# Kernel optimization log

Measured on AMD Instinct MI355X. Metric: run time of the kernel, lower is better.

Reference implementation:

```python
import jax, jax.numpy as jnp
import numpy as np

B, N, QD = 2, 2048, 1024
HEADS, DIM_HEAD = 16, 64
INNER = HEADS * DIM_HEAD  # 1024
SCALE = DIM_HEAD ** -0.5


def setup_inputs() -> dict:
    key = jax.random.key(0)
    ks = jax.random.split(key, 8)
    x = jax.random.normal(ks[0], (B, N, QD), dtype=jnp.float32)
    bias = jax.random.normal(ks[1], (B, N, N), dtype=jnp.float32)
    mask = jax.random.randint(ks[2], (B, N), 0, 2) > 0
    # parameters (nn.Linear stores weight [out, in]; we keep [in, out] and matmul x @ W)
    Wq = jax.random.normal(ks[3], (QD, INNER), dtype=jnp.float32) * (QD ** -0.5)
    Wkv = jax.random.normal(ks[4], (QD, 2 * INNER), dtype=jnp.float32) * (QD ** -0.5)
    Wo = jax.random.normal(ks[5], (INNER, QD), dtype=jnp.float32) * (INNER ** -0.5)
    bo = jax.random.normal(ks[6], (QD,), dtype=jnp.float32) * 0.01
    return {"x": x, "bias": bias, "mask": mask, "Wq": Wq, "Wkv": Wkv, "Wo": Wo, "bo": bo}


def reference(x, bias, mask, Wq, Wkv, Wo, bo):
    b, n, _ = x.shape
    q = x @ Wq                      # [b, n, inner]
    kv = x @ Wkv                    # [b, n, 2*inner] (context defaults to x)
    k, v = jnp.split(kv, 2, axis=-1)
    # split heads: [b, h, n, d]
    split = lambda t: t.reshape(b, n, HEADS, DIM_HEAD).transpose(0, 2, 1, 3)
    q, k, v = split(q), split(k), split(v)
    sim = jnp.einsum('bhid,bhjd->bhij', q, k) * SCALE   # [b, h, n, n]
    sim = sim + bias[:, None, :, :]                      # additive bias broadcast over heads
    max_neg = -jnp.finfo(sim.dtype).max
    sim = jnp.where(mask[:, None, None, :], sim, max_neg)  # per-key mask
    attn = jax.nn.softmax(sim, axis=-1)
    out = jnp.einsum('bhij,bhjd->bhid', attn, v)         # [b, h, n, d]
    out = out.transpose(0, 2, 1, 3).reshape(b, n, INNER)  # merge heads
    return out @ Wo + bo
```

## Files before the change

### kernel.cpp

```cpp
#include <hip/hip_runtime.h>
#include <hip/hip_bf16.h>
#include <stdint.h>

#define B_     2
#define N_     2048
#define QD_    1024
#define H_     16
#define DH_    64
#define INNER_ 1024
#define SCALE_ 0.125f

typedef unsigned short u16;
typedef __attribute__((ext_vector_type(8))) short bf16x8;
typedef __attribute__((ext_vector_type(4))) float f32x4;
typedef __attribute__((ext_vector_type(4))) unsigned short u16x4;
typedef __attribute__((ext_vector_type(8))) unsigned short u16x8;

#define GLD16(gp, lp) __builtin_amdgcn_global_load_lds( \
    (const __attribute__((address_space(1))) unsigned int*)(gp), \
    (__attribute__((address_space(3))) unsigned int*)(lp), 16, 0, 0)

__device__ inline u16 f2bf(float f) {
    union { float f; uint32_t u; } c; c.f = f;
    uint32_t r = c.u + 0x7FFFu + ((c.u >> 16) & 1u);
    return (u16)(r >> 16);
}
__device__ inline float bf2f(u16 s) {
    union { uint32_t u; float f; } c; c.u = ((uint32_t)s) << 16;
    return c.f;
}
__device__ inline void split2(float v, u16 &h, u16 &l) {
    u16 hs = f2bf(v);
    h = hs;
    l = f2bf(v - bf2f(hs));
}
__device__ inline unsigned pk2(float a, float b) {
    float2 f; f.x = a; f.y = b;
    union { __hip_bfloat162 v; unsigned u; } c;
    c.v = __float22bfloat162_rn(f);
    return c.u;
}
__device__ inline float f4get(const float4& v, int r) {
    return r == 0 ? v.x : r == 1 ? v.y : r == 2 ? v.z : v.w;
}

__global__ __launch_bounds__(256) void prep_kernel(
    const float* __restrict__ x, u16* __restrict__ xh, u16* __restrict__ xl,
    const float* __restrict__ Wq, const float* __restrict__ Wkv, const float* __restrict__ Wo,
    u16* __restrict__ wTh, u16* __restrict__ wTl,
    u16* __restrict__ woTh, u16* __restrict__ woTl)
{
    __shared__ float t[32][33];
    const int blk = blockIdx.x, tid = threadIdx.x;
    if (blk < 4096) {
        int idx = blk * 256 + tid;
        float4 v = ((const float4*)x)[idx];
        u16x4 hv, lv; u16 h, l;
        split2(v.x, h, l); hv.x = h; lv.x = l;
        split2(v.y, h, l); hv.y = h; lv.y = l;
        split2(v.z, h, l); hv.z = h; lv.z = l;
        split2(v.w, h, l); hv.w = h; lv.w = l;
        ((u16x4*)xh)[idx] = hv;
        ((u16x4*)xl)[idx] = lv;
        return;
    }
    int local = blk - 4096;
    const float* src; u16 *dhi, *dlo; int C, bx, by;
    if (local < 1024)      { src = Wq;  dhi = wTh;                dlo = wTl;                C = 1024; by = local >> 5; bx = local & 31; }
    else if (local < 3072) { int l2 = local - 1024; src = Wkv; dhi = wTh + 1024 * 1024; dlo = wTl + 1024 * 1024; C = 2048; by = l2 >> 6; bx = l2 & 63; }
    else                   { int l2 = local - 3072; src = Wo;  dhi = woTh;               dlo = woTl;               C = 1024; by = l2 >> 5; bx = l2 & 31; }
    const int x0 = bx * 32, y0 = by * 32;
    const int tx = tid & 31, ty = tid >> 5;
    for (int yy = ty; yy < 32; yy += 8)
        t[yy][tx] = src[(size_t)(y0 + yy) * C + x0 + tx];
    __syncthreads();
    for (int i = ty; i < 32; i += 8) {
        float v = t[tx][i];
        u16 h, l; split2(v, h, l);
        size_t o = (size_t)(x0 + i) * 1024 + y0 + tx;
        dhi[o] = h; dlo[o] = l;
    }
}

__device__ inline void bias_read(int T, int bkoff, int bl16,
                                 const float* __restrict__ bias,
                                 const int* __restrict__ mask,
                                 float4 bR[4], int4& bM)
{
    int bb2 = T >> 10, rest = T & 1023;
    int k0b = (rest & 31) * 64, q0 = (rest >> 5) * 64;
    int kk = k0b + bkoff;
    bM = *(const int4*)&mask[bb2 * N_ + kk];
#pragma unroll
    for (int m = 0; m < 4; m++)
        bR[m] = *(const float4*)&bias[((size_t)bb2 * N_ + q0 + m * 16 + bl16) * N_ + kk];
}
__device__ inline void bias_store(int T, int bwvr, int blane, int bhf,
                                  const float4 bR[4], const int4& bM,
                                  u16* __restrict__ bsw)
{
    int bb2 = T >> 10, rest = T & 1023;
    int k0b = (rest & 31) * 64, q0 = (rest >> 5) * 64;
    int wv = ((k0b >> 5) & 3) + bwvr;
    const u16 NEG = f2bf(-1e30f);
    const int mok[4] = { bM.x, bM.y, bM.z, bM.w };
    u16x8 o0, o1;
#pragma unroll
    for (int i = 0; i < 8; i++) {
        int m = i >> 2, r = i & 3;
        o0[i] = mok[r] ? f2bf(f4get(bR[m], r)) : NEG;
    }
#pragma unroll
    for (int i = 0; i < 8; i++) {
        int m = 2 + (i >> 2), r = i & 3;
        o1[i] = mok[r] ? f2bf(f4get(bR[m], r)) : NEG;
    }
    size_t ob = ((((size_t)bb2 * 32 + (q0 >> 6)) * 16 + (k0b >> 7)) * 4 + wv) * 2048
                + (size_t)blane * 32 + bhf * 16;
    *(u16x8*)&bsw[ob]     = o0;
    *(u16x8*)&bsw[ob + 8] = o1;
}

__global__ __launch_bounds__(256) void bias_kernel(
    const float* __restrict__ bias, const int* __restrict__ mask,
    u16* __restrict__ bsw)
{
    const int bid = blockIdx.x, tid = threadIdx.x;
    const int bp = tid >> 1, bhf = tid & 1;
    const int blane = bp & 63, bquad = blane >> 4, bl16 = blane & 15;
    const int bwvr = bp >> 6;
    const int bkoff = bwvr * 32 + bquad * 8 + bhf * 4;
    float4 bR[4]; int4 bM;
    bias_read(bid, bkoff, bl16, bias, mask, bR, bM);
    bias_store(bid, bwvr, blane, bhf, bR, bM, bsw);
}

__global__ __launch_bounds__(256) void gemm_qkv(
    const u16* __restrict__ Ah, const u16* __restrict__ Al,
    const u16* __restrict__ Bh,
    u16* __restrict__ qh,
    u16* __restrict__ kb, u16* __restrict__ vT)
{
    __shared__ __align__(16) char smem[49152];
    const int tid = threadIdx.x;
    const int gid = blockIdx.x;

    const int wave = tid >> 6, lane = tid & 63;
    const int quad = lane >> 4, l16 = lane & 15;
    const int wm = wave >> 1, wn = wave & 1;
    const int bx = gid % 24, by = gid / 24;
    const int bm = by * 128, bn = bx * 128;
    const bool comp = (bx < 8);

    f32x4 acc[4][4];
#pragma unroll
    for (int i = 0; i < 4; i++)
#pragma unroll
        for (int j = 0; j < 4; j++) acc[i][j] = (f32x4){0.f, 0.f, 0.f, 0.f};

    const int row0 = tid >> 2, g4 = tid & 3;
    const int r1 = row0, r2 = row0 + 64;
    const int gc1 = (g4 ^ (r1 & 3)) * 8, gc2 = (g4 ^ (r2 & 3)) * 8;
    const size_t a1 = (size_t)(bm + r1) * 1024 + gc1, a2 = (size_t)(bm + r2) * 1024 + gc2;
    const size_t b1 = (size_t)(bn + r1) * 1024 + gc1, b2 = (size_t)(bn + r2) * 1024 + gc2;
    const int ldsw = wave * 1024;

    auto issue = [&](char* base, int kn) {
        GLD16(Ah + a1 + kn, base + ldsw);
        GLD16(Ah + a2 + kn, base + 4096 + ldsw);
        GLD16(Bh + b1 + kn, base + 16384 + ldsw);
        GLD16(Bh + b2 + kn, base + 20480 + ldsw);
        if (comp) {
            GLD16(Al + a1 + kn, base + 8192 + ldsw);
            GLD16(Al + a2 + kn, base + 12288 + ldsw);
        }
    };

    issue(smem, 0);
    int cur = 0;
    for (int k0 = 0; k0 < 1024; k0 += 32) {
        __syncthreads();
        char* cb_ = smem + cur * 24576;
        if (k0 + 32 < 1024) issue(smem + (cur ^ 1) * 24576, k0 + 32);
        const u16* cAh = (const u16*)cb_;
        const u16* cAl = (const u16*)(cb_ + 8192);
        const u16* cBh = (const u16*)(cb_ + 16384);
        bf16x8 fah[4], fal[4], fbh[4];
#pragma unroll
        for (int s = 0; s < 4; s++) {
            int ra = wm * 64 + s * 16 + l16;
            int rb = wn * 64 + s * 16 + l16;
            int ca = (quad ^ (ra & 3)) * 8;
            int cb = (quad ^ (rb & 3)) * 8;
            fah[s] = *(const bf16x8*)&cAh[ra * 32 + ca];
            fbh[s] = *(const bf16x8*)&cBh[rb * 32 + cb];
            if (comp) fal[s] = *(const bf16x8*)&cAl[ra * 32 + ca];
        }
#pragma unroll
        for (int sm = 0; sm < 4; sm++)
#pragma unroll
            for (int sn = 0; sn < 4; sn++) {
                acc[sm][sn] = __builtin_amdgcn_mfma_f32_16x16x32_bf16(fah[sm], fbh[sn], acc[sm][sn], 0, 0, 0);
                if (comp)
                    acc[sm][sn] = __builtin_amdgcn_mfma_f32_16x16x32_bf16(fal[sm], fbh[sn], acc[sm][sn], 0, 0, 0);
            }
        cur ^= 1;
    }
#pragma unroll
    for (int sm = 0; sm < 4; sm++) {
        int rowb = bm + wm * 64 + sm * 16 + quad * 4;
        int bb = rowb >> 11, i0 = rowb & 2047;
#pragma unroll
        for (int sn = 0; sn < 4; sn++) {
            int col = bn + wn * 64 + sn * 16 + l16;
            int region = col >> 10;
            int hh = (col >> 6) & 15;
            int d = col & 63;
            if (region == 0) {
#pragma unroll
                for (int r = 0; r < 4; r++) {
                    size_t o = (((size_t)(bb * H_ + hh)) * N_ + i0 + r) * DH_ + d;
                    qh[o] = f2bf(acc[sm][sn][r] * SCALE_);
                }
            } else if (region == 1) {
#pragma unroll
                for (int r = 0; r < 4; r++) {
                    size_t o = (((size_t)(bb * H_ + hh)) * N_ + i0 + r) * DH_ + d;
                    kb[o] = f2bf(acc[sm][sn][r]);
                }
            } else {
                u16x4 pv;
#pragma unroll
                for (int r = 0; r < 4; r++) pv[r] = f2bf(acc[sm][sn][r]);
                *(u16x4*)&vT[(((size_t)(bb * H_ + hh)) * DH_ + d) * N_ + i0] = pv;
            }
        }
    }
}

__global__ __launch_bounds__(256) void gemm_out(
    const u16* __restrict__ Ab,
    const u16* __restrict__ Bh,
    const float* __restrict__ bo, float* __restrict__ out)
{
    __shared__ __align__(16) char smem[24576];
    const int tid = threadIdx.x;
    const int wave = tid >> 6, lane = tid & 63;
    const int quad = lane >> 4, l16 = lane & 15;
    const int wm = wave >> 1, wn = wave & 1;
    const int bm = blockIdx.y * 128, bn = blockIdx.x * 64;

    f32x4 acc[4][2];
#pragma unroll
    for (int i = 0; i < 4; i++)
#pragma unroll
        for (int j = 0; j < 2; j++) acc[i][j] = (f32x4){0.f, 0.f, 0.f, 0.f};

    const int row0 = tid >> 2, g4 = tid & 3;
    const int r1 = row0, r2 = row0 + 64;
    const int gc1 = (g4 ^ (r1 & 3)) * 8, gc2 = (g4 ^ (r2 & 3)) * 8;
    const size_t a1 = (size_t)(bm + r1) * 1024 + gc1, a2 = (size_t)(bm + r2) * 1024 + gc2;
    const size_t bgo = (size_t)(bn + r1) * 1024 + gc1;
    const int ldsw = wave * 1024;

    auto issue = [&](char* base, int kn) {
        GLD16(Ab + a1 + kn, base + ldsw);
        GLD16(Ab + a2 + kn, base + 4096 + ldsw);
        GLD16(Bh + bgo + kn, base + 8192 + ldsw);
    };

    issue(smem, 0);
    int cur = 0;
    for (int k0 = 0; k0 < 1024; k0 += 32) {
        __syncthreads();
        char* cb_ = smem + cur * 12288;
        if (k0 + 32 < 1024) issue(smem + (cur ^ 1) * 12288, k0 + 32);
        const u16* cA  = (const u16*)cb_;
        const u16* cBh = (const u16*)(cb_ + 8192);
        bf16x8 fa[4], fbh[2];
#pragma unroll
        for (int s = 0; s < 4; s++) {
            int ra = wm * 64 + s * 16 + l16;
            int ca = (quad ^ (ra & 3)) * 8;
            fa[s] = *(const bf16x8*)&cA[ra * 32 + ca];
        }
#pragma unroll
        for (int s = 0; s < 2; s++) {
            int rb = wn * 32 + s * 16 + l16;
            int cb = (quad ^ (rb & 3)) * 8;
            fbh[s] = *(const bf16x8*)&cBh[rb * 32 + cb];
        }
#pragma unroll
        for (int sm = 0; sm < 4; sm++)
#pragma unroll
            for (int sn = 0; sn < 2; sn++)
                acc[sm][sn] = __builtin_amdgcn_mfma_f32_16x16x32_bf16(fa[sm], fbh[sn], acc[sm][sn], 0, 0, 0);
        cur ^= 1;
    }
#pragma unroll
    for (int sm = 0; sm < 4; sm++) {
        int rowb = bm + wm * 64 + sm * 16 + quad * 4;
#pragma unroll
        for (int sn = 0; sn < 2; sn++) {
            int col = bn + wn * 32 + sn * 16 + l16;
            float bv = bo[col];
#pragma unroll
            for (int r = 0; r < 4; r++)
                out[(size_t)(rowb + r) * 1024 + col] = acc[sm][sn][r] + bv;
        }
    }
}

#define LDK 72
#define LDV 128

__global__ __launch_bounds__(256, 2) void attn_kernel(
    const u16* __restrict__ qh,
    const u16* __restrict__ kb, const u16* __restrict__ vT,
    const u16* __restrict__ bsw, u16* __restrict__ ob)
{
    __shared__ __align__(16) char smem[35328];
    u16* sK  = (u16*)smem;
    u16* sVt = (u16*)(smem + 18432);
    float* rO = (float*)smem;
    float* rL = (float*)(smem + 34816);

    const int bh = blockIdx.y, b = bh >> 4, h = bh & 15;
    const int qt = blockIdx.x, qbase = qt * 64;
    const int tid = threadIdx.x, wave = tid >> 6, lane = tid & 63;
    const int quad = lane >> 4, l16 = lane & 15;

    bf16x8 aq[4][2];
#pragma unroll
    for (int m = 0; m < 4; m++) {
        size_t qo = ((size_t)bh * N_ + qbase + m * 16 + l16) * DH_ + quad * 8;
        aq[m][0] = *(const bf16x8*)&qh[qo];
        aq[m][1] = *(const bf16x8*)&qh[qo + 32];
    }
    f32x4 Oacc[4][4], lacc[4];
#pragma unroll
    for (int m = 0; m < 4; m++) {
        lacc[m] = (f32x4){0.f, 0.f, 0.f, 0.f};
#pragma unroll
        for (int nd = 0; nd < 4; nd++) Oacc[m][nd] = (f32x4){0.f, 0.f, 0.f, 0.f};
    }
    bf16x8 ones;
#pragma unroll
    for (int i = 0; i < 8; i++) ones[i] = (short)0x3F80;

    const int rK = tid >> 3, cK = (tid & 7) * 8;
    const int sigK = ((rK & 4) << 2) + ((rK >> 3) << 2) + (rK & 3);
    const int rV = tid >> 4;
    const int vg = tid & 15;
    const int cV = vg * 8;
    const int vsw = (vg ^ (rV & 7)) * 8;
    const int vrg = ((wave * 4 + quad) ^ (l16 & 7)) * 8;
    const size_t kgbase = (size_t)bh * N_ * DH_;
    const size_t vgbase = (size_t)bh * DH_ * N_;
    const size_t bswb = (size_t)(b * 32 + qt) * 131072 + (size_t)wave * 2048
                        + (size_t)lane * 32;

    bf16x8 pK[4], pV[4];
    u16x8 cB[4], nB[4];
#pragma unroll
    for (int it = 0; it < 4; it++) {
        pK[it] = *(const bf16x8*)&kb[kgbase + (size_t)(rK + it * 32) * DH_ + cK];
        pV[it] = *(const bf16x8*)&vT[vgbase + (size_t)(rV + it * 16) * N_ + cV];
    }
#pragma unroll
    for (int c = 0; c < 4; c++) cB[c] = *(const u16x8*)&bsw[bswb + c * 8];

    for (int jt = 0; jt < 16; jt++) {
#pragma unroll
        for (int it = 0; it < 4; it++) {
            *(bf16x8*)&sK[(it * 32 + sigK) * LDK + cK] = pK[it];
            *(bf16x8*)&sVt[(rV + it * 16) * LDV + vsw] = pV[it];
        }
        __syncthreads();
        {
            int jn = (jt + 1) & 15;
            int j0n = jn * 128;
#pragma unroll
            for (int it = 0; it < 4; it++) {
                pK[it] = *(const bf16x8*)&kb[kgbase + (size_t)(j0n + rK + it * 32) * DH_ + cK];
                pV[it] = *(const bf16x8*)&vT[vgbase + (size_t)(rV + it * 16) * N_ + j0n + cV];
            }
            size_t bb = bswb + (size_t)jn * 8192;
#pragma unroll
            for (int c = 0; c < 4; c++) nB[c] = *(const u16x8*)&bsw[bb + c * 8];
        }
        bf16x8 kf[2][2], vf[4];
#pragma unroll
        for (int n = 0; n < 2; n++)
#pragma unroll
            for (int s = 0; s < 2; s++)
                kf[n][s] = *(const bf16x8*)&sK[(wave * 32 + n * 16 + l16) * LDK + s * 32 + quad * 8];
#pragma unroll
        for (int nd = 0; nd < 4; nd++)
            vf[nd] = *(const bf16x8*)&sVt[(nd * 16 + l16) * LDV + vrg];

#pragma unroll
        for (int m = 0; m < 4; m++) {
            f32x4 S0 = (f32x4){0.f, 0.f, 0.f, 0.f};
            f32x4 S1 = (f32x4){0.f, 0.f, 0.f, 0.f};
#pragma unroll
            for (int s = 0; s < 2; s++) {
                S0 = __builtin_amdgcn_mfma_f32_16x16x32_bf16(kf[0][s], aq[m][s], S0, 0, 0, 0);
                S1 = __builtin_amdgcn_mfma_f32_16x16x32_bf16(kf[1][s], aq[m][s], S1, 0, 0, 0);
            }
            float p0[4], p1[4];
#pragma unroll
            for (int r = 0; r < 4; r++) {
                p0[r] = __expf(S0[r] + bf2f(cB[m >> 1][(m & 1) * 4 + r]));
                p1[r] = __expf(S1[r] + bf2f(cB[2 + (m >> 1)][(m & 1) * 4 + r]));
            }
            union { bf16x8 v; unsigned w[4]; } pa;
            pa.w[0] = pk2(p0[0], p0[1]);
            pa.w[1] = pk2(p0[2], p0[3]);
            pa.w[2] = pk2(p1[0], p1[1]);
            pa.w[3] = pk2(p1[2], p1[3]);
            lacc[m] = __builtin_amdgcn_mfma_f32_16x16x32_bf16(pa.v, ones, lacc[m], 0, 0, 0);
#pragma unroll
            for (int nd = 0; nd < 4; nd++)
                Oacc[m][nd] = __builtin_amdgcn_mfma_f32_16x16x32_bf16(pa.v, vf[nd], Oacc[m][nd], 0, 0, 0);
        }
#pragma unroll
        for (int c = 0; c < 4; c++) cB[c] = nB[c];
        __syncthreads();
    }

    if (wave >= 2) {
        int slot = wave - 2;
#pragma unroll
        for (int m = 0; m < 4; m++) {
#pragma unroll
            for (int nd = 0; nd < 4; nd++)
#pragma unroll
                for (int r = 0; r < 4; r++)
                    rO[(slot * 64 + m * 16 + quad * 4 + r) * 68 + nd * 16 + l16] = Oacc[m][nd][r];
            if (l16 == 0)
#pragma unroll
                for (int r = 0; r < 4; r++)
                    rL[slot * 64 + m * 16 + quad * 4 + r] = lacc[m][r];
        }
    }
    __syncthreads();
    if (wave < 2) {
        int slot = wave;
#pragma unroll
        for (int m = 0; m < 4; m++) {
#pragma unroll
            for (int nd = 0; nd < 4; nd++)
#pragma unroll
                for (int r = 0; r < 4; r++) {
                    int idx = (slot * 64 + m * 16 + quad * 4 + r) * 68 + nd * 16 + l16;
                    rO[idx] += Oacc[m][nd][r];
                }
            if (l16 == 0)
#pragma unroll
                for (int r = 0; r < 4; r++)
                    rL[slot * 64 + m * 16 + quad * 4 + r] += lacc[m][r];
        }
    }
    __syncthreads();
    {
        const int q = tid >> 2, dg = (tid & 3) * 16;
        float l = rL[q] + rL[64 + q];
        float inv = 1.f / l;
        f32x4 s[4];
#pragma unroll
        for (int i4 = 0; i4 < 4; i4++) {
            s[i4] = *(const f32x4*)&rO[(size_t)q * 68 + dg + i4 * 4];
            f32x4 v = *(const f32x4*)&rO[(size_t)(64 + q) * 68 + dg + i4 * 4];
            s[i4] += v;
        }
        size_t obase = ((size_t)b * N_ + qbase + q) * INNER_ + h * 64 + dg;
#pragma unroll
        for (int i4 = 0; i4 < 4; i4++) {
            u16x4 o4;
#pragma unroll
            for (int r = 0; r < 4; r++) o4[r] = f2bf(s[i4][r] * inv);
            *(u16x4*)&ob[obase + i4 * 4] = o4;
        }
    }
}

extern "C" void kernel_launch(void* const* d_in, const int* in_sizes, int n_in,
                              void* d_out, int out_size, void* d_ws, size_t ws_size,
                              hipStream_t stream)
{
    const float* x    = (const float*)d_in[0];
    const float* bias = (const float*)d_in[1];
    const int*   mask = (const int*)d_in[2];
    const float* Wq   = (const float*)d_in[3];
    const float* Wkv  = (const float*)d_in[4];
    const float* Wo   = (const float*)d_in[5];
    const float* bo   = (const float*)d_in[6];
    float* out = (float*)d_out;

    char* w = (char*)d_ws;
    const size_t MB = 1024 * 1024;
    u16* q_h   = (u16*)(w);
    u16* k_b   = (u16*)(w + 16 * MB);
    u16* v_T   = (u16*)(w + 24 * MB);
    u16* xs_h  = (u16*)(w + 32 * MB);
    u16* xs_l  = (u16*)(w + 40 * MB);
    u16* wT_h  = (u16*)(w + 48 * MB);
    u16* wT_l  = (u16*)(w + 54 * MB);
    u16* woT_h = (u16*)(w + 60 * MB);
    u16* woT_l = (u16*)(w + 62 * MB);
    u16* o_b   = (u16*)(w + 64 * MB);

    const size_t bsw_bytes = (size_t)2 * N_ * N_ * sizeof(u16);
    const bool concurrent = ws_size >= 72 * MB + bsw_bytes;

    u16* bsw = concurrent ? (u16*)(w + 72 * MB) : (u16*)(w + 32 * MB);

    prep_kernel<<<8192, 256, 0, stream>>>(x, xs_h, xs_l, Wq, Wkv, Wo, wT_h, wT_l, woT_h, woT_l);
    gemm_qkv<<<768, 256, 0, stream>>>(xs_h, xs_l, wT_h, q_h, k_b, v_T);
    bias_kernel<<<2048, 256, 0, stream>>>(bias, mask, bsw);
    attn_kernel<<<dim3(32, 32), 256, 0, stream>>>(q_h, k_b, v_T, bsw, o_b);
    gemm_out<<<dim3(16, 32), 256, 0, stream>>>(o_b, woT_h, bo, out);
}
```

Baseline: 269.5 us.

## Fuse bias prep into prep kernel and remap attention grid per XCD

When the workspace is large enough, the bias/mask conversion blocks are appended to the prep kernel, which removes one kernel launch and lets that work run alongside the input and weight splitting. The attention grid is flattened to 1D and remapped so each XCD handles four consecutive (batch, head) pairs, which should improve L2 reuse of K/V. The last iteration no longer prefetches a wrapped-around tile. In exchange the prep kernel gets longer, and the remapping assumes round-robin block dispatch across 8 XCDs.

Result: no change. 270.3 us (+0.3%).

```diff
diff --git a/kernel.cpp b/kernel.cpp
--- a/kernel.cpp
+++ b/kernel.cpp
@@ -44,14 +44,72 @@
     return r == 0 ? v.x : r == 1 ? v.y : r == 2 ? v.z : v.w;
 }
 
+__device__ inline void bias_read(int T, int bkoff, int bl16,
+                                 const float* __restrict__ bias,
+                                 const int* __restrict__ mask,
+                                 float4 bR[4], int4& bM)
+{
+    int bb2 = T >> 10, rest = T & 1023;
+    int k0b = (rest & 31) * 64, q0 = (rest >> 5) * 64;
+    int kk = k0b + bkoff;
+    bM = *(const int4*)&mask[bb2 * N_ + kk];
+#pragma unroll
+    for (int m = 0; m < 4; m++)
+        bR[m] = *(const float4*)&bias[((size_t)bb2 * N_ + q0 + m * 16 + bl16) * N_ + kk];
+}
+__device__ inline void bias_store(int T, int bwvr, int blane, int bhf,
+                                  const float4 bR[4], const int4& bM,
+                                  u16* __restrict__ bsw)
+{
+    int bb2 = T >> 10, rest = T & 1023;
+    int k0b = (rest & 31) * 64, q0 = (rest >> 5) * 64;
+    int wv = ((k0b >> 5) & 3) + bwvr;
+    const u16 NEG = f2bf(-1e30f);
+    const int mok[4] = { bM.x, bM.y, bM.z, bM.w };
+    u16x8 o0, o1;
+#pragma unroll
+    for (int i = 0; i < 8; i++) {
+        int m = i >> 2, r = i & 3;
+        o0[i] = mok[r] ? f2bf(f4get(bR[m], r)) : NEG;
+    }
+#pragma unroll
+    for (int i = 0; i < 8; i++) {
+        int m = 2 + (i >> 2), r = i & 3;
+        o1[i] = mok[r] ? f2bf(f4get(bR[m], r)) : NEG;
+    }
+    size_t ob = ((((size_t)bb2 * 32 + (q0 >> 6)) * 16 + (k0b >> 7)) * 4 + wv) * 2048
+                + (size_t)blane * 32 + bhf * 16;
+    *(u16x8*)&bsw[ob]     = o0;
+    *(u16x8*)&bsw[ob + 8] = o1;
+}
+__device__ inline void bias_block(int T, int tid,
+                                  const float* __restrict__ bias,
+                                  const int* __restrict__ mask,
+                                  u16* __restrict__ bsw)
+{
+    const int bp = tid >> 1, bhf = tid & 1;
+    const int blane = bp & 63, bquad = blane >> 4, bl16 = blane & 15;
+    const int bwvr = bp >> 6;
+    const int bkoff = bwvr * 32 + bquad * 8 + bhf * 4;
+    float4 bR[4]; int4 bM;
+    bias_read(T, bkoff, bl16, bias, mask, bR, bM);
+    bias_store(T, bwvr, blane, bhf, bR, bM, bsw);
+}
+
 __global__ __launch_bounds__(256) void prep_kernel(
     const float* __restrict__ x, u16* __restrict__ xh, u16* __restrict__ xl,
     const float* __restrict__ Wq, const float* __restrict__ Wkv, const float* __restrict__ Wo,
     u16* __restrict__ wTh, u16* __restrict__ wTl,
-    u16* __restrict__ woTh, u16* __restrict__ woTl)
+    u16* __restrict__ woTh, u16* __restrict__ woTl,
+    const float* __restrict__ bias, const int* __restrict__ mask,
+    u16* __restrict__ bsw)
 {
     __shared__ float t[32][33];
     const int blk = blockIdx.x, tid = threadIdx.x;
+    if (blk >= 8192) {
+        bias_block(blk - 8192, tid, bias, mask, bsw);
+        return;
+    }
     if (blk < 4096) {
         int idx = blk * 256 + tid;
         float4 v = ((const float4*)x)[idx];
@@ -82,57 +140,11 @@
     }
 }
 
-__device__ inline void bias_read(int T, int bkoff, int bl16,
-                                 const float* __restrict__ bias,
-                                 const int* __restrict__ mask,
-                                 float4 bR[4], int4& bM)
-{
-    int bb2 = T >> 10, rest = T & 1023;
-    int k0b = (rest & 31) * 64, q0 = (rest >> 5) * 64;
-    int kk = k0b + bkoff;
-    bM = *(const int4*)&mask[bb2 * N_ + kk];
-#pragma unroll
-    for (int m = 0; m < 4; m++)
-        bR[m] = *(const float4*)&bias[((size_t)bb2 * N_ + q0 + m * 16 + bl16) * N_ + kk];
-}
-__device__ inline void bias_store(int T, int bwvr, int blane, int bhf,
-                                  const float4 bR[4], const int4& bM,
-                                  u16* __restrict__ bsw)
-{
-    int bb2 = T >> 10, rest = T & 1023;
-    int k0b = (rest & 31) * 64, q0 = (rest >> 5) * 64;
-    int wv = ((k0b >> 5) & 3) + bwvr;
-    const u16 NEG = f2bf(-1e30f);
-    const int mok[4] = { bM.x, bM.y, bM.z, bM.w };
-    u16x8 o0, o1;
-#pragma unroll
-    for (int i = 0; i < 8; i++) {
-        int m = i >> 2, r = i & 3;
-        o0[i] = mok[r] ? f2bf(f4get(bR[m], r)) : NEG;
-    }
-#pragma unroll
-    for (int i = 0; i < 8; i++) {
-        int m = 2 + (i >> 2), r = i & 3;
-        o1[i] = mok[r] ? f2bf(f4get(bR[m], r)) : NEG;
-    }
-    size_t ob = ((((size_t)bb2 * 32 + (q0 >> 6)) * 16 + (k0b >> 7)) * 4 + wv) * 2048
-                + (size_t)blane * 32 + bhf * 16;
-    *(u16x8*)&bsw[ob]     = o0;
-    *(u16x8*)&bsw[ob + 8] = o1;
-}
-
 __global__ __launch_bounds__(256) void bias_kernel(
     const float* __restrict__ bias, const int* __restrict__ mask,
     u16* __restrict__ bsw)
 {
-    const int bid = blockIdx.x, tid = threadIdx.x;
-    const int bp = tid >> 1, bhf = tid & 1;
-    const int blane = bp & 63, bquad = blane >> 4, bl16 = blane & 15;
-    const int bwvr = bp >> 6;
-    const int bkoff = bwvr * 32 + bquad * 8 + bhf * 4;
-    float4 bR[4]; int4 bM;
-    bias_read(bid, bkoff, bl16, bias, mask, bR, bM);
-    bias_store(bid, bwvr, blane, bhf, bR, bM, bsw);
+    bias_block(blockIdx.x, threadIdx.x, bias, mask, bsw);
 }
 
 __global__ __launch_bounds__(256) void gemm_qkv(
@@ -325,8 +337,12 @@
     float* rO = (float*)smem;
     float* rL = (float*)(smem + 34816);
 
-    const int bh = blockIdx.y, b = bh >> 4, h = bh & 15;
-    const int qt = blockIdx.x, qbase = qt * 64;
+    const int lin = blockIdx.x;
+    const int xcd = lin & 7, slot = lin >> 3;
+    const int bh = xcd * 4 + (slot >> 5);
+    const int qt = slot & 31;
+    const int b = bh >> 4, h = bh & 15;
+    const int qbase = qt * 64;
     const int tid = threadIdx.x, wave = tid >> 6, lane = tid & 63;
     const int quad = lane >> 4, l16 = lane & 15;
 
@@ -377,15 +393,14 @@
             *(bf16x8*)&sVt[(rV + it * 16) * LDV + vsw] = pV[it];
         }
         __syncthreads();
-        {
-            int jn = (jt + 1) & 15;
-            int j0n = jn * 128;
+        if (jt < 15) {
+            int j0n = (jt + 1) * 128;
 #pragma unroll
             for (int it = 0; it < 4; it++) {
                 pK[it] = *(const bf16x8*)&kb[kgbase + (size_t)(j0n + rK + it * 32) * DH_ + cK];
                 pV[it] = *(const bf16x8*)&vT[vgbase + (size_t)(rV + it * 16) * N_ + j0n + cV];
             }
-            size_t bb = bswb + (size_t)jn * 8192;
+            size_t bb = bswb + (size_t)(jt + 1) * 8192;
 #pragma unroll
             for (int c = 0; c < 4; c++) nB[c] = *(const u16x8*)&bsw[bb + c * 8];
         }
@@ -430,36 +445,36 @@
     }
 
     if (wave >= 2) {
-        int slot = wave - 2;
+        int slot2 = wave - 2;
 #pragma unroll
         for (int m = 0; m < 4; m++) {
 #pragma unroll
             for (int nd = 0; nd < 4; nd++)
 #pragma unroll
                 for (int r = 0; r < 4; r++)
-                    rO[(slot * 64 + m * 16 + quad * 4 + r) * 68 + nd * 16 + l16] = Oacc[m][nd][r];
+                    rO[(slot2 * 64 + m * 16 + quad * 4 + r) * 68 + nd * 16 + l16] = Oacc[m][nd][r];
             if (l16 == 0)
 #pragma unroll
                 for (int r = 0; r < 4; r++)
-                    rL[slot * 64 + m * 16 + quad * 4 + r] = lacc[m][r];
+                    rL[slot2 * 64 + m * 16 + quad * 4 + r] = lacc[m][r];
         }
     }
     __syncthreads();
     if (wave < 2) {
-        int slot = wave;
+        int slot2 = wave;
 #pragma unroll
         for (int m = 0; m < 4; m++) {
 #pragma unroll
             for (int nd = 0; nd < 4; nd++)
 #pragma unroll
                 for (int r = 0; r < 4; r++) {
-                    int idx = (slot * 64 + m * 16 + quad * 4 + r) * 68 + nd * 16 + l16;
+                    int idx = (slot2 * 64 + m * 16 + quad * 4 + r) * 68 + nd * 16 + l16;
                     rO[idx] += Oacc[m][nd][r];
                 }
             if (l16 == 0)
 #pragma unroll
                 for (int r = 0; r < 4; r++)
-                    rL[slot * 64 + m * 16 + quad * 4 + r] += lacc[m][r];
+                    rL[slot2 * 64 + m * 16 + quad * 4 + r] += lacc[m][r];
         }
     }
     __syncthreads();
@@ -514,11 +529,21 @@
     const size_t bsw_bytes = (size_t)2 * N_ * N_ * sizeof(u16);
     const bool concurrent = ws_size >= 72 * MB + bsw_bytes;
 
-    u16* bsw = concurrent ? (u16*)(w + 72 * MB) : (u16*)(w + 32 * MB);
-
-    prep_kernel<<<8192, 256, 0, stream>>>(x, xs_h, xs_l, Wq, Wkv, Wo, wT_h, wT_l, woT_h, woT_l);
-    gemm_qkv<<<768, 256, 0, stream>>>(xs_h, xs_l, wT_h, q_h, k_b, v_T);
-    bias_kernel<<<2048, 256, 0, stream>>>(bias, mask, bsw);
-    attn_kernel<<<dim3(32, 32), 256, 0, stream>>>(q_h, k_b, v_T, bsw, o_b);
+    if (concurrent) {
+        u16* bsw = (u16*)(w + 72 * MB);
+        prep_kernel<<<10240, 256, 0, stream>>>(x, xs_h, xs_l, Wq, Wkv, Wo,
+                                               wT_h, wT_l, woT_h, woT_l,
+                                               bias, mask, bsw);
+        gemm_qkv<<<768, 256, 0, stream>>>(xs_h, xs_l, wT_h, q_h, k_b, v_T);
+        attn_kernel<<<1024, 256, 0, stream>>>(q_h, k_b, v_T, bsw, o_b);
+    } else {
+        u16* bsw = (u16*)(w + 32 * MB);
+        prep_kernel<<<8192, 256, 0, stream>>>(x, xs_h, xs_l, Wq, Wkv, Wo,
+                                              wT_h, wT_l, woT_h, woT_l,
+                                              bias, mask, bsw);
+        gemm_qkv<<<768, 256, 0, stream>>>(xs_h, xs_l, wT_h, q_h, k_b, v_T);
+        bias_kernel<<<2048, 256, 0, stream>>>(bias, mask, bsw);
+        attn_kernel<<<1024, 256, 0, stream>>>(q_h, k_b, v_T, bsw, o_b);
+    }
     gemm_out<<<dim3(16, 32), 256, 0, stream>>>(o_b, woT_h, bo, out);
 }
```
